# Kernel optimization log

Hardware: AMD Instinct MI355X
Metric: run time of the kernel (lower is better)

The kernel has to match this reference:

```python
import jax, jax.numpy as jnp
import numpy as np

N_NODES = 50000


def _gcn_conv(x, W, b, src, dst, n):
    # PyG GCNConv: h = x @ W, symmetric-normalized aggregation, then + bias.
    h = x @ W  # [N, out]
    deg = jax.ops.segment_sum(jnp.ones_like(dst, dtype=h.dtype), dst, num_segments=n)
    dinv = jnp.where(deg > 0, jax.lax.rsqrt(jnp.maximum(deg, 1e-12)), 0.0)
    norm = dinv[src] * dinv[dst]  # [E]
    msg = h[src] * norm[:, None]  # gather + scale, [E, out]
    out = jax.ops.segment_sum(msg, dst, num_segments=n)
    return out + b


def setup_inputs() -> dict:
    key = jax.random.key(0)
    ks = jax.random.split(key, 8)
    d_in, d_h, d_out = 256, 256, 128
    E = 800000
    x = jax.random.normal(ks[0], (N_NODES, d_in), dtype=jnp.float32)
    edge_index = jax.random.randint(ks[1], (2, E), 0, N_NODES, dtype=jnp.int64)
    def glorot(k, shape):
        lim = np.sqrt(6.0 / (shape[0] + shape[1]))
        return jax.random.uniform(k, shape, jnp.float32, -lim, lim)
    return {
        "x": x,
        "edge_index": edge_index,
        "W1": glorot(ks[2], (d_in, d_h)), "b1": jnp.zeros((d_h,), jnp.float32),
        "W2": glorot(ks[3], (d_h, d_h)), "b2": jnp.zeros((d_h,), jnp.float32),
        "W3": glorot(ks[4], (d_h, d_out)), "b3": jnp.zeros((d_out,), jnp.float32),
    }


def reference(x, edge_index, W1, b1, W2, b2, W3, b3):
    n = x.shape[0]
    # add self-loops once (PyG GCNConv default add_self_loops=True)
    loop = jnp.arange(n, dtype=edge_index.dtype)
    src = jnp.concatenate([edge_index[0], loop])
    dst = jnp.concatenate([edge_index[1], loop])
    h = _gcn_conv(x, W1, b1, src, dst, n)
    h = jax.nn.relu(h)  # dropout is identity in eval mode
    h = _gcn_conv(h, W2, b2, src, dst, n)
    h = jax.nn.relu(h)
    h = _gcn_conv(h, W3, b3, src, dst, n)
    return h
```

## Files before the change

### kernel.cpp

```cpp
#include <hip/hip_runtime.h>
#include <stdint.h>

typedef short v8s __attribute__((ext_vector_type(8)));
typedef float v4f __attribute__((ext_vector_type(4)));
typedef float v2f __attribute__((ext_vector_type(2)));

__device__ inline float bf2f(unsigned short h) {
    union { unsigned u; float f; } c; c.u = ((unsigned)h) << 16; return c.f;
}
__device__ inline unsigned short f2bf(float f) {
    union { float f; unsigned u; } c; c.f = f;
    unsigned u = c.u;
    unsigned r = (u + 0x7FFFu + ((u >> 16) & 1u)) >> 16;
    return (unsigned short)r;
}
__device__ inline void gl_lds16(const unsigned short* g, unsigned short* l) {
    __builtin_amdgcn_global_load_lds(
        (const __attribute__((address_space(1))) unsigned int*)(g),
        (__attribute__((address_space(3))) unsigned int*)(l), 16, 0, 0);
}

__global__ void k_pre1(const int* __restrict__ dst, int E,
                       int* __restrict__ cnt, int* __restrict__ seq,
                       const float* __restrict__ W1, const float* __restrict__ W2,
                       const float* __restrict__ W3, unsigned short* __restrict__ Wt,
                       int gE) {
    int b = blockIdx.x;
    if (b < gE) {
        int e = b * 256 + threadIdx.x;
        if (e < E) seq[e] = atomicAdd(&cnt[dst[e]], 1);
    } else {
        int idx = (b - gE) * 256 + threadIdx.x;
        const float* W; int base, N;
        if (idx < 65536)       { W = W1; base = 0;      N = 256; }
        else if (idx < 131072) { W = W2; base = 65536;  N = 256; }
        else                   { W = W3; base = 131072; N = 128; }
        int loc = idx - base;
        int nn = loc >> 8;
        int k = loc & 255;
        Wt[idx] = f2bf(W[(size_t)k * N + nn]);
    }
}

__global__ void k_scan1(const int* __restrict__ cnt, int n, int* __restrict__ incl,
                        int* __restrict__ bsum) {
    __shared__ int sm[256];
    int t = threadIdx.x;
    int i = blockIdx.x * 256 + t;
    int v = (i < n) ? cnt[i] : 0;
    sm[t] = v; __syncthreads();
    for (int off = 1; off < 256; off <<= 1) {
        int add = (t >= off) ? sm[t - off] : 0;
        __syncthreads();
        sm[t] += add;
        __syncthreads();
    }
    if (i < n) incl[i] = sm[t];
    if (t == 255) bsum[blockIdx.x] = sm[255];
}

__global__ void k_scan23(const int* __restrict__ cnt, int n,
                         const int* __restrict__ bsum,
                         int* __restrict__ rs, float* __restrict__ dinv) {
    __shared__ int red[256];
    int t = threadIdx.x;
    int acc = 0;
    for (int j = t; j < (int)blockIdx.x; j += 256) acc += bsum[j];
    red[t] = acc; __syncthreads();
    for (int s = 128; s > 0; s >>= 1) {
        if (t < s) red[t] += red[t + s];
        __syncthreads();
    }
    int boff = red[0];
    int i = blockIdx.x * 256 + t;
    if (i < n) {
        int c = cnt[i];
        rs[i] = rs[i] + boff - c;
        dinv[i] = rsqrtf((float)(c + 1));
    }
}

__global__ void k_scatter2(const int* __restrict__ src, const int* __restrict__ dst,
                           const int* __restrict__ seq, int E,
                           const int* __restrict__ rs, int* __restrict__ col) {
    int e = blockIdx.x * 256 + threadIdx.x;
    if (e < E) col[rs[dst[e]] + seq[e]] = src[e];
}

__launch_bounds__(256, 4)
__global__ void k_gemm(const unsigned short* __restrict__ A,
                       const unsigned short* __restrict__ Wt,
                       unsigned short* __restrict__ Hs,
                       const float* __restrict__ dinv, int n, int N) {
    __shared__ unsigned short sA[128 * 32];
    __shared__ unsigned short sB[128 * 32];
    const int t = threadIdx.x;
    const int lane = t & 63;
    const int wave = t >> 6;
    const int wm = wave >> 1, wn = wave & 1;
    const int m0 = blockIdx.x * 128;
    const int n0 = blockIdx.y * 128;

    v4f acc[4][4];
#pragma unroll
    for (int i = 0; i < 4; i++)
#pragma unroll
        for (int j = 0; j < 4; j++)
#pragma unroll
            for (int r = 0; r < 4; r++) acc[i][j][r] = 0.f;

    const int c0 = t, c1 = t + 256;
    const int r0 = c0 >> 2, kc0 = (c0 & 3) * 8;
    const int r1 = c1 >> 2, kc1 = (c1 & 3) * 8;
    const size_t aBase0 = (size_t)(m0 + r0) * 256 + kc0;
    const size_t aBase1 = (size_t)(m0 + r1) * 256 + kc1;
    const size_t bBase0 = (size_t)(n0 + r0) * 256 + kc0;
    const size_t bBase1 = (size_t)(n0 + r1) * 256 + kc1;

    const int q = lane >> 4;
    const int lm = lane & 15;

    for (int k0 = 0; k0 < 256; k0 += 32) {
        __syncthreads();
        gl_lds16(A + aBase0 + k0, &sA[c0 * 8]);
        gl_lds16(A + aBase1 + k0, &sA[c1 * 8]);
        gl_lds16(Wt + bBase0 + k0, &sB[c0 * 8]);
        gl_lds16(Wt + bBase1 + k0, &sB[c1 * 8]);
        __syncthreads();

        v8s afr[4], bfr[4];
#pragma unroll
        for (int i = 0; i < 4; i++) {
            int r = wm * 64 + i * 16 + lm;
            afr[i] = *(const v8s*)&sA[r * 32 + q * 8];
        }
#pragma unroll
        for (int j = 0; j < 4; j++) {
            int nn = wn * 64 + j * 16 + lm;
            bfr[j] = *(const v8s*)&sB[nn * 32 + q * 8];
        }
#pragma unroll
        for (int i = 0; i < 4; i++)
#pragma unroll
            for (int j = 0; j < 4; j++)
                acc[i][j] = __builtin_amdgcn_mfma_f32_16x16x32_bf16(afr[i], bfr[j],
                                                                    acc[i][j], 0, 0, 0);
    }

#pragma unroll
    for (int i = 0; i < 4; i++) {
        int mbase = m0 + wm * 64 + i * 16 + q * 4;
#pragma unroll
        for (int r = 0; r < 4; r++) {
            int m = mbase + r;
            float s = (m < n) ? dinv[m] : 0.f;
#pragma unroll
            for (int j = 0; j < 4; j++) {
                int colI = n0 + wn * 64 + j * 16 + lm;
                Hs[(size_t)m * N + colI] = f2bf(acc[i][j][r] * s);
            }
        }
    }
}

__launch_bounds__(256, 4)
__global__ void k_gemm_x(const float* __restrict__ x,
                         const unsigned short* __restrict__ Wt,
                         unsigned short* __restrict__ Hs,
                         const float* __restrict__ dinv, int n, int N) {
    __shared__ unsigned short sA[128 * 32];
    __shared__ unsigned short sB[128 * 32];
    const int t = threadIdx.x;
    const int lane = t & 63;
    const int wave = t >> 6;
    const int wm = wave >> 1, wn = wave & 1;
    const int m0 = blockIdx.x * 128;
    const int n0 = blockIdx.y * 128;

    v4f acc[4][4];
#pragma unroll
    for (int i = 0; i < 4; i++)
#pragma unroll
        for (int j = 0; j < 4; j++)
#pragma unroll
            for (int r = 0; r < 4; r++) acc[i][j][r] = 0.f;

    const int c0 = t, c1 = t + 256;
    const int r0 = c0 >> 2, kc0 = (c0 & 3) * 8;
    const int r1 = c1 >> 2, kc1 = (c1 & 3) * 8;
    const int ra0 = min(m0 + r0, n - 1);
    const int ra1 = min(m0 + r1, n - 1);
    const float* ax0 = x + (size_t)ra0 * 256 + kc0;
    const float* ax1 = x + (size_t)ra1 * 256 + kc1;
    const size_t bBase0 = (size_t)(n0 + r0) * 256 + kc0;
    const size_t bBase1 = (size_t)(n0 + r1) * 256 + kc1;

    const int q = lane >> 4;
    const int lm = lane & 15;

    for (int k0 = 0; k0 < 256; k0 += 32) {
        __syncthreads();
        float4 u0 = *(const float4*)(ax0 + k0);
        float4 u1 = *(const float4*)(ax0 + k0 + 4);
        float4 u2 = *(const float4*)(ax1 + k0);
        float4 u3 = *(const float4*)(ax1 + k0 + 4);
        gl_lds16(Wt + bBase0 + k0, &sB[c0 * 8]);
        gl_lds16(Wt + bBase1 + k0, &sB[c1 * 8]);
        v8s w0, w1;
        w0[0] = (short)f2bf(u0.x); w0[1] = (short)f2bf(u0.y);
        w0[2] = (short)f2bf(u0.z); w0[3] = (short)f2bf(u0.w);
        w0[4] = (short)f2bf(u1.x); w0[5] = (short)f2bf(u1.y);
        w0[6] = (short)f2bf(u1.z); w0[7] = (short)f2bf(u1.w);
        w1[0] = (short)f2bf(u2.x); w1[1] = (short)f2bf(u2.y);
        w1[2] = (short)f2bf(u2.z); w1[3] = (short)f2bf(u2.w);
        w1[4] = (short)f2bf(u3.x); w1[5] = (short)f2bf(u3.y);
        w1[6] = (short)f2bf(u3.z); w1[7] = (short)f2bf(u3.w);
        *(v8s*)&sA[c0 * 8] = w0;
        *(v8s*)&sA[c1 * 8] = w1;
        __syncthreads();

        v8s afr[4], bfr[4];
#pragma unroll
        for (int i = 0; i < 4; i++) {
            int r = wm * 64 + i * 16 + lm;
            afr[i] = *(const v8s*)&sA[r * 32 + q * 8];
        }
#pragma unroll
        for (int j = 0; j < 4; j++) {
            int nn = wn * 64 + j * 16 + lm;
            bfr[j] = *(const v8s*)&sB[nn * 32 + q * 8];
        }
#pragma unroll
        for (int i = 0; i < 4; i++)
#pragma unroll
            for (int j = 0; j < 4; j++)
                acc[i][j] = __builtin_amdgcn_mfma_f32_16x16x32_bf16(afr[i], bfr[j],
                                                                    acc[i][j], 0, 0, 0);
    }

#pragma unroll
    for (int i = 0; i < 4; i++) {
        int mbase = m0 + wm * 64 + i * 16 + q * 4;
#pragma unroll
        for (int r = 0; r < 4; r++) {
            int m = mbase + r;
            float s = (m < n) ? dinv[m] : 0.f;
#pragma unroll
            for (int j = 0; j < 4; j++) {
                int colI = n0 + wn * 64 + j * 16 + lm;
                Hs[(size_t)m * N + colI] = f2bf(acc[i][j][r] * s);
            }
        }
    }
}

template <int D, bool RELU, bool F32OUT>
__launch_bounds__(256, 8)
__global__ void k_agg(const unsigned short* __restrict__ Hs,
                      const int* __restrict__ rs, const int* __restrict__ cnt,
                      const int* __restrict__ col, const float* __restrict__ dinv,
                      const float* __restrict__ bias,
                      unsigned short* __restrict__ outb, float* __restrict__ outf,
                      int n, int nzero) {
    constexpr int LPN = D / 8;
    constexpr int NPG = 64 / LPN;
    const int lane = threadIdx.x & 63;
    const int i = blockIdx.x * 4 + (threadIdx.x >> 6);
    if (i >= n) return;
    const int g = lane / LPN;
    const int cl = lane % LPN;

    v2f acc[4];
#pragma unroll
    for (int k = 0; k < 4; k++) acc[k] = (v2f){0.f, 0.f};

    auto accq = [&](unsigned u, int k) {
        union { unsigned uu; float f; } lo, hi;
        lo.uu = u << 16;
        hi.uu = u & 0xffff0000u;
        v2f t; t[0] = lo.f; t[1] = hi.f;
        acc[k] += t;
    };
    auto acc16 = [&](uint4 q) { accq(q.x, 0); accq(q.y, 1); accq(q.z, 2); accq(q.w, 3); };

    const unsigned short* base = Hs + cl * 8;
    const int s = rs[i], deg = cnt[i];
    const int T = deg + 1;
    const int Tpad = (T + NPG - 1) & ~(NPG - 1);

    for (int b = 0; b < Tpad; b += 64) {
        int t = b + lane;
        int v;
        if (t == 0) v = i;
        else if (t <= deg) v = col[s + t - 1];
        else v = nzero;
        int lim = min(64, Tpad - b);
        int t2 = 0;
        for (; t2 + 4 * NPG <= lim; t2 += 4 * NPG) {
            int c0 = __shfl(v, t2 + 0 * NPG + g);
            int c1 = __shfl(v, t2 + 1 * NPG + g);
            int c2 = __shfl(v, t2 + 2 * NPG + g);
            int c3 = __shfl(v, t2 + 3 * NPG + g);
            uint4 q0 = *(const uint4*)(base + (size_t)c0 * D);
            uint4 q1 = *(const uint4*)(base + (size_t)c1 * D);
            uint4 q2 = *(const uint4*)(base + (size_t)c2 * D);
            uint4 q3 = *(const uint4*)(base + (size_t)c3 * D);
            acc16(q0); acc16(q1); acc16(q2); acc16(q3);
        }
        for (; t2 + NPG <= lim; t2 += NPG) {
            int c0 = __shfl(v, t2 + g);
            uint4 q0 = *(const uint4*)(base + (size_t)c0 * D);
            acc16(q0);
        }
    }

#pragma unroll
    for (int off = LPN; off < 64; off <<= 1) {
#pragma unroll
        for (int k = 0; k < 4; k++) {
            acc[k][0] += __shfl_xor(acc[k][0], off);
            acc[k][1] += __shfl_xor(acc[k][1], off);
        }
    }

    if (g == 0) {
        float di = dinv[i];
        float o[8];
#pragma unroll
        for (int k = 0; k < 4; k++) {
            o[2 * k + 0] = di * acc[k][0] + bias[cl * 8 + 2 * k + 0];
            o[2 * k + 1] = di * acc[k][1] + bias[cl * 8 + 2 * k + 1];
        }
        if (RELU) {
#pragma unroll
            for (int k = 0; k < 8; k++) o[k] = fmaxf(o[k], 0.f);
        }
        if constexpr (F32OUT) {
            float* p = outf + (size_t)i * D + cl * 8;
            *(float4*)p = make_float4(o[0], o[1], o[2], o[3]);
            *(float4*)(p + 4) = make_float4(o[4], o[5], o[6], o[7]);
        } else {
            uint4 q;
            q.x = ((unsigned)f2bf(o[1]) << 16) | f2bf(o[0]);
            q.y = ((unsigned)f2bf(o[3]) << 16) | f2bf(o[2]);
            q.z = ((unsigned)f2bf(o[5]) << 16) | f2bf(o[4]);
            q.w = ((unsigned)f2bf(o[7]) << 16) | f2bf(o[6]);
            *(uint4*)(outb + (size_t)i * D + cl * 8) = q;
        }
    }
}

extern "C" void kernel_launch(void* const* d_in, const int* in_sizes, int n_in,
                              void* d_out, int out_size, void* d_ws, size_t ws_size,
                              hipStream_t stream) {
    const float* x  = (const float*)d_in[0];
    const int*   ei = (const int*)d_in[1];
    const float* W1 = (const float*)d_in[2];
    const float* b1 = (const float*)d_in[3];
    const float* W2 = (const float*)d_in[4];
    const float* b2 = (const float*)d_in[5];
    const float* W3 = (const float*)d_in[6];
    const float* b3 = (const float*)d_in[7];

    const int n = in_sizes[0] / 256;
    const int E = in_sizes[1] / 2;
    const int mpad = ((n + 127) / 128) * 128;

    char* ws = (char*)d_ws;
    size_t off = 0;
    auto alloc = [&](size_t bytes) -> void* {
        void* p = ws + off;
        off += (bytes + 255) & ~(size_t)255;
        return p;
    };
    int* cnt      = (int*)alloc((size_t)n * 4);
    int* rs       = (int*)alloc((size_t)n * 4);
    float* dinv   = (float*)alloc((size_t)n * 4);
    int* bsum     = (int*)alloc(256 * 4);
    int* seq      = (int*)alloc((size_t)E * 4);
    int* col      = (int*)alloc((size_t)E * 4);
    unsigned short* Wt = (unsigned short*)alloc((size_t)163840 * 2);
    unsigned short* W1t = Wt;
    unsigned short* W2t = Wt + 65536;
    unsigned short* W3t = Wt + 131072;
    unsigned short* bufA = (unsigned short*)alloc((size_t)mpad * 256 * 2);
    unsigned short* bufB = (unsigned short*)alloc((size_t)mpad * 256 * 2);
    (void)ws_size; (void)n_in; (void)out_size;

    const int* srcp = ei;
    const int* dstp = ei + E;
    const int gE = (E + 255) / 256;
    const int gN = (n + 255) / 256;
    const int gW = 640;
    const int nmb = mpad / 128;

    hipMemsetAsync(cnt, 0, (size_t)n * 4, stream);

    k_pre1<<<gE + gW, 256, 0, stream>>>(dstp, E, cnt, seq, W1, W2, W3, Wt, gE);
    k_scan1<<<gN, 256, 0, stream>>>(cnt, n, rs, bsum);
    k_scan23<<<gN, 256, 0, stream>>>(cnt, n, bsum, rs, dinv);
    k_scatter2<<<gE, 256, 0, stream>>>(srcp, dstp, seq, E, rs, col);

    const int gAgg = (n + 3) / 4;
    dim3 gg1(nmb, 2);
    k_gemm_x<<<gg1, 256, 0, stream>>>(x, W1t, bufB, dinv, n, 256);
    k_agg<256, true, false><<<gAgg, 256, 0, stream>>>(bufB, rs, cnt, col, dinv, b1,
                                                      bufA, nullptr, n, n);
    k_gemm<<<gg1, 256, 0, stream>>>(bufA, W2t, bufB, dinv, n, 256);
    k_agg<256, true, false><<<gAgg, 256, 0, stream>>>(bufB, rs, cnt, col, dinv, b2,
                                                      bufA, nullptr, n, n);
    dim3 gg3(nmb, 1);
    k_gemm<<<gg3, 256, 0, stream>>>(bufA, W3t, bufB, dinv, n, 128);
    k_agg<128, false, true><<<gAgg, 256, 0, stream>>>(bufB, rs, cnt, col, dinv, b3,
                                                      nullptr, (float*)d_out, n, n);
}
```

Baseline: 356.1 us.

## Fuse CSR-build preprocessing into one cooperative kernel with grid syncs

Replaces the memset plus four preprocessing kernels (count, two-level scan, scatter) with a single cooperative kernel of 1024 blocks, separated by grid-wide syncs. This removes several kernel launches and the gaps between them. In exchange it adds grid.sync overhead and uses grid-stride loops with a fixed block count. The scan assumes at most 256 chunks (n up to 65536), which holds for 50000 nodes.

```diff
diff --git a/kernel.cpp b/kernel.cpp
--- a/kernel.cpp
+++ b/kernel.cpp
@@ -1,5 +1,8 @@
 #include <hip/hip_runtime.h>
+#include <hip/hip_cooperative_groups.h>
 #include <stdint.h>
+
+namespace cg = cooperative_groups;
 
 typedef short v8s __attribute__((ext_vector_type(8)));
 typedef float v4f __attribute__((ext_vector_type(4)));
@@ -20,17 +23,24 @@
         (__attribute__((address_space(3))) unsigned int*)(l), 16, 0, 0);
 }
 
-__global__ void k_pre1(const int* __restrict__ dst, int E,
+__global__ void k_coop(const int* __restrict__ src, const int* __restrict__ dst, int E,
                        int* __restrict__ cnt, int* __restrict__ seq,
+                       int* __restrict__ rs, float* __restrict__ dinv,
+                       int* __restrict__ col, int n, int nChunks,
                        const float* __restrict__ W1, const float* __restrict__ W2,
                        const float* __restrict__ W3, unsigned short* __restrict__ Wt,
-                       int gE) {
-    int b = blockIdx.x;
-    if (b < gE) {
-        int e = b * 256 + threadIdx.x;
-        if (e < E) seq[e] = atomicAdd(&cnt[dst[e]], 1);
-    } else {
-        int idx = (b - gE) * 256 + threadIdx.x;
+                       int* __restrict__ csum) {
+    cg::grid_group grid = cg::this_grid();
+    __shared__ int sm[256];
+    const int t = threadIdx.x;
+    const int gtid = blockIdx.x * 256 + t;
+    const int gsz = gridDim.x * 256;
+
+    for (int i = gtid; i < n; i += gsz) cnt[i] = 0;
+    grid.sync();
+
+    for (int e = gtid; e < E; e += gsz) seq[e] = atomicAdd(&cnt[dst[e]], 1);
+    for (int idx = gtid; idx < 163840; idx += gsz) {
         const float* W; int base, N;
         if (idx < 65536)       { W = W1; base = 0;      N = 256; }
         else if (idx < 131072) { W = W2; base = 65536;  N = 256; }
@@ -40,51 +50,45 @@
         int k = loc & 255;
         Wt[idx] = f2bf(W[(size_t)k * N + nn]);
     }
-}
-
-__global__ void k_scan1(const int* __restrict__ cnt, int n, int* __restrict__ incl,
-                        int* __restrict__ bsum) {
-    __shared__ int sm[256];
-    int t = threadIdx.x;
-    int i = blockIdx.x * 256 + t;
-    int v = (i < n) ? cnt[i] : 0;
-    sm[t] = v; __syncthreads();
-    for (int off = 1; off < 256; off <<= 1) {
-        int add = (t >= off) ? sm[t - off] : 0;
-        __syncthreads();
-        sm[t] += add;
-        __syncthreads();
-    }
-    if (i < n) incl[i] = sm[t];
-    if (t == 255) bsum[blockIdx.x] = sm[255];
-}
-
-__global__ void k_scan23(const int* __restrict__ cnt, int n,
-                         const int* __restrict__ bsum,
-                         int* __restrict__ rs, float* __restrict__ dinv) {
-    __shared__ int red[256];
-    int t = threadIdx.x;
-    int acc = 0;
-    for (int j = t; j < (int)blockIdx.x; j += 256) acc += bsum[j];
-    red[t] = acc; __syncthreads();
-    for (int s = 128; s > 0; s >>= 1) {
-        if (t < s) red[t] += red[t + s];
-        __syncthreads();
-    }
-    int boff = red[0];
-    int i = blockIdx.x * 256 + t;
-    if (i < n) {
-        int c = cnt[i];
-        rs[i] = rs[i] + boff - c;
-        dinv[i] = rsqrtf((float)(c + 1));
-    }
-}
-
-__global__ void k_scatter2(const int* __restrict__ src, const int* __restrict__ dst,
-                           const int* __restrict__ seq, int E,
-                           const int* __restrict__ rs, int* __restrict__ col) {
-    int e = blockIdx.x * 256 + threadIdx.x;
-    if (e < E) col[rs[dst[e]] + seq[e]] = src[e];
+    grid.sync();
+
+    for (int c = blockIdx.x; c < nChunks; c += gridDim.x) {
+        int i = c * 256 + t;
+        sm[t] = (i < n) ? cnt[i] : 0; __syncthreads();
+        for (int s = 128; s > 0; s >>= 1) {
+            if (t < s) sm[t] += sm[t + s];
+            __syncthreads();
+        }
+        if (t == 0) csum[c] = sm[0];
+        __syncthreads();
+    }
+    grid.sync();
+
+    for (int c = blockIdx.x; c < nChunks; c += gridDim.x) {
+        sm[t] = (t < c) ? csum[t] : 0; __syncthreads();
+        for (int s = 128; s > 0; s >>= 1) {
+            if (t < s) sm[t] += sm[t + s];
+            __syncthreads();
+        }
+        int boff = sm[0]; __syncthreads();
+        int i = c * 256 + t;
+        int v = (i < n) ? cnt[i] : 0;
+        sm[t] = v; __syncthreads();
+        for (int off = 1; off < 256; off <<= 1) {
+            int a = (t >= off) ? sm[t - off] : 0;
+            __syncthreads();
+            sm[t] += a;
+            __syncthreads();
+        }
+        if (i < n) {
+            rs[i] = boff + sm[t] - v;
+            dinv[i] = rsqrtf((float)(v + 1));
+        }
+        __syncthreads();
+    }
+    grid.sync();
+
+    for (int e = gtid; e < E; e += gsz) col[rs[dst[e]] + seq[e]] = src[e];
 }
 
 __launch_bounds__(256, 4)
@@ -362,8 +366,8 @@
     const float* W3 = (const float*)d_in[6];
     const float* b3 = (const float*)d_in[7];
 
-    const int n = in_sizes[0] / 256;
-    const int E = in_sizes[1] / 2;
+    int n = in_sizes[0] / 256;
+    int E = in_sizes[1] / 2;
     const int mpad = ((n + 127) / 128) * 128;
 
     char* ws = (char*)d_ws;
@@ -376,7 +380,7 @@
     int* cnt      = (int*)alloc((size_t)n * 4);
     int* rs       = (int*)alloc((size_t)n * 4);
     float* dinv   = (float*)alloc((size_t)n * 4);
-    int* bsum     = (int*)alloc(256 * 4);
+    int* csum     = (int*)alloc(256 * 4);
     int* seq      = (int*)alloc((size_t)E * 4);
     int* col      = (int*)alloc((size_t)E * 4);
     unsigned short* Wt = (unsigned short*)alloc((size_t)163840 * 2);
@@ -389,17 +393,15 @@
 
     const int* srcp = ei;
     const int* dstp = ei + E;
-    const int gE = (E + 255) / 256;
-    const int gN = (n + 255) / 256;
-    const int gW = 640;
+    int nChunks = (n + 255) / 256;
     const int nmb = mpad / 128;
 
-    hipMemsetAsync(cnt, 0, (size_t)n * 4, stream);
-
-    k_pre1<<<gE + gW, 256, 0, stream>>>(dstp, E, cnt, seq, W1, W2, W3, Wt, gE);
-    k_scan1<<<gN, 256, 0, stream>>>(cnt, n, rs, bsum);
-    k_scan23<<<gN, 256, 0, stream>>>(cnt, n, bsum, rs, dinv);
-    k_scatter2<<<gE, 256, 0, stream>>>(srcp, dstp, seq, E, rs, col);
+    void* cargs[] = {
+        (void*)&srcp, (void*)&dstp, (void*)&E, (void*)&cnt, (void*)&seq,
+        (void*)&rs, (void*)&dinv, (void*)&col, (void*)&n, (void*)&nChunks,
+        (void*)&W1, (void*)&W2, (void*)&W3, (void*)&Wt, (void*)&csum,
+    };
+    hipLaunchCooperativeKernel((void*)k_coop, dim3(1024), dim3(256), cargs, 0, stream);
 
     const int gAgg = (n + 3) / 4;
     dim3 gg1(nmb, 2);
```

Measured after the change: 743.7 us. 109% more time.
